# Kernel tuning notes

Measured on AMD Instinct MI355X. Metric: run time of the kernel, lower is better.

The kernel has to match this reference:

```python
import jax, jax.numpy as jnp
import numpy as np

WS = 3          # windows_size
ND = 3          # num_dilation, dilations [1,2,3]
NSTATE = 16     # d_state
RANK = 12       # dt_rank = ceil(192/16)
TOPK = 36       # max(1,(20//3)**2)*depth
DM = 192        # d_model
DI = 384        # d_inner = 2*d_model
B0, HH, WW = 8, 96, 96


def setup_inputs() -> dict:
    ks = jax.random.split(jax.random.key(0), 12)
    f = jax.random.normal
    return {
        "x": f(ks[0], (B0, HH, WW, DM), jnp.float32),
        "W_in": f(ks[1], (2 * DI, DM), jnp.float32) * 0.02,
        "conv_w": f(ks[2], (DI, 1, 7, 7), jnp.float32) * 0.05,
        "conv_b": f(ks[3], (DI,), jnp.float32) * 0.01,
        "x_proj_w": f(ks[4], (2, RANK + 2 * NSTATE, DI), jnp.float32) * 0.02,
        "dt_w": f(ks[5], (2, DI, RANK), jnp.float32) * 0.02,
        "dt_b": f(ks[6], (2, DI), jnp.float32) * 0.01,
        "A_logs": jnp.tile(jnp.log(jnp.arange(1, NSTATE + 1, dtype=jnp.float32)), (2 * DI, 1)),
        "Ds": jnp.ones((2 * DI,), jnp.float32),
        "W_kv": f(ks[7], (2 * DI, DI), jnp.float32) * 0.02,
        "b_kv": jnp.zeros((2 * DI,), jnp.float32),
        "ln_g": jnp.ones((DI,), jnp.float32),
        "ln_b": jnp.zeros((DI,), jnp.float32),
        "W_out": f(ks[8], (DM, DI), jnp.float32) * 0.02,
    }


def _selective_scan(xs, x_proj_w, dt_w, dt_b, A_logs, Ds):
    # xs: (B, K=2, D, L) -> (B, K, D, L). Standard Mamba selective scan.
    B, K, D, L = xs.shape
    x_dbl = jnp.einsum('bkdl,kcd->bkcl', xs, x_proj_w)          # (B,K,R+2N,L)
    dts = x_dbl[:, :, :RANK]
    Bs = x_dbl[:, :, RANK:RANK + NSTATE]                        # (B,K,N,L)
    Cs = x_dbl[:, :, RANK + NSTATE:]                            # (B,K,N,L)
    delta = jax.nn.softplus(jnp.einsum('bkrl,kdr->bkdl', dts, dt_w) + dt_b[None, :, :, None])
    A = -jnp.exp(A_logs).reshape(K, D, NSTATE)
    dA = jnp.exp(delta[..., None] * A[None, :, :, None, :])    # (B,K,D,L,N)
    dBu = delta[..., None] * Bs.transpose(0, 1, 3, 2)[:, :, None, :, :] * xs[..., None]
    dA = jnp.moveaxis(dA, 3, 0)                                 # (L,B,K,D,N)
    dBu = jnp.moveaxis(dBu, 3, 0)
    C = jnp.moveaxis(Cs, 3, 0)                                  # (L,B,K,N)

    def step(h, inp):
        dA_t, dBu_t, C_t = inp
        h = dA_t * h + dBu_t
        y = jnp.einsum('bkdn,bkn->bkd', h, C_t)
        return h, y

    h0 = jnp.zeros((B, K, D, NSTATE), xs.dtype)
    _, ys = jax.lax.scan(step, h0, (dA, dBu, C))                # ys: (L,B,K,D)
    y = jnp.moveaxis(ys, 0, 3)                                  # (B,K,D,L)
    return y + Ds.reshape(1, K, D, 1) * xs


def _dynamic_mask_active(x):
    # x: (B,D,H,W). Partition into WSxWS windows, keep TOPK by mean activation.
    B, D, H, W = x.shape
    nH, nW = H // WS, W // WS
    w = x.reshape(B, D, nH, WS, nW, WS).transpose(0, 2, 4, 1, 3, 5)
    w = w.reshape(B, nH * nW, D, WS * WS)                       # (B,nWin,D,ws2)
    score = w.mean(axis=(2, 3))                                 # (B,nWin)
    _, idx = jax.lax.top_k(score, TOPK)                         # (B,TOPK)
    g = jnp.take_along_axis(w, idx[:, :, None, None], axis=1)   # (B,TOPK,D,ws2)
    return g.transpose(0, 2, 1, 3).reshape(B, D, TOPK * WS * WS)


def _unfold(x, d):
    # torch nn.Unfold(kernel=WS, dilation=d, padding=d, stride=1) on (B,C,H,W)
    B, C, H, W = x.shape
    xp = jnp.pad(x, ((0, 0), (0, 0), (d, d), (d, d)))
    pats = [xp[:, :, i * d:i * d + H, j * d:j * d + W] for i in range(WS) for j in range(WS)]
    p = jnp.stack(pats, axis=2)                                 # (B,C,ws2,H,W) channel-major like torch
    return p.reshape(B, C, WS * WS, H * W)


def _forward(x, W_in, conv_w, conv_b, x_proj_w, dt_w, dt_b, A_logs, Ds,
             W_kv, b_kv, ln_g, ln_b, W_out):
    B, H, W_, _ = x.shape
    xz = jnp.einsum('bhwc,oc->bhwo', x, W_in)
    xf, z = jnp.split(xz, 2, axis=-1)                           # (B,H,W,DI) each
    xc = xf.transpose(0, 3, 1, 2)
    xc = jax.lax.conv_general_dilated(xc, conv_w, (1, 1), [(3, 3), (3, 3)],
                                      feature_group_count=conv_w.shape[0],
                                      dimension_numbers=('NCHW', 'OIHW', 'NCHW'))
    xc = xc + conv_b[None, :, None, None]                       # (B,DI,H,W)
    D = xc.shape[1]

    # foreground SSM on active windows (forward + flipped scan)
    act = _dynamic_mask_active(xc)                              # (B,D,L)
    xs = jnp.stack([act, jnp.flip(act, axis=-1)], axis=1)       # (B,2,D,L)
    out = _selective_scan(xs, x_proj_w, dt_w, dt_b, A_logs, Ds)
    y1 = out[:, 0] + jnp.flip(out[:, 1], axis=-1)               # (B,D,L)
    y1 = y1.transpose(0, 2, 1)                                  # (B,L,D)

    L = y1.shape[1]
    ws2 = WS * WS
    n2 = L // ws2
    kv = jnp.einsum('bld,od->blo', y1, W_kv) + b_kv             # (B,L,2D)
    hd = 2 * D // ND
    t = kv.reshape(B, n2, ws2, ND, hd).transpose(3, 0, 4, 2, 1)  # (ND,B,hd,ws2,n2)
    Q, Kt = t[:, :, :hd // 2], t[:, :, hd // 2:]                 # (ND,B,D/ND,ws2,n2)

    dch = D // ND
    xr = xc.reshape(B, ND, dch, H, W_)
    ys = []
    for i in range(ND):
        V = _unfold(xr[:, i], i + 1)                            # (B,dch,ws2,n1)
        V = V.transpose(0, 1, 3, 2)                             # (B,dch,n1,ws2)
        s = jnp.einsum('bcwn,bcwn->bcw', Q[i], Kt[i]) / np.sqrt(dch).astype(np.float32)
        # softmax over a singleton axis (as in the source) -> all ones
        A_M = jax.nn.softmax(s[..., None], axis=-1)[..., 0]     # (B,dch,ws2)
        ys.append(jnp.einsum('bcnw,bcw->bcn', V, A_M))          # (B,dch,n1)
    y = jnp.concatenate(ys, axis=1)                             # (B,D,n1)
    y = y.transpose(0, 2, 1)                                    # (B,n1,D)

    mu = y.mean(-1, keepdims=True)
    var = y.var(-1, keepdims=True)
    y = (y - mu) / jnp.sqrt(var + 1e-5) * ln_g + ln_b
    y = y.reshape(B, H, W_, D) + z
    return jnp.einsum('bhwd,od->bhwo', y, W_out)


def reference(x, W_in, conv_w, conv_b, x_proj_w, dt_w, dt_b, A_logs, Ds,
              W_kv, b_kv, ln_g, ln_b, W_out):
    return _forward(x, W_in, conv_w, conv_b, x_proj_w, dt_w, dt_b, A_logs, Ds,
                    W_kv, b_kv, ln_g, ln_b, W_out)
```

## Files before the change

kernel.cpp:

```cpp
#include <hip/hip_runtime.h>
#include <cstddef>

#define B0V 8
#define HSV 96
#define WSV 96
#define DMV 192
#define DIV 384
#define MTOT (B0V*HSV*WSV)

typedef __attribute__((ext_vector_type(8))) unsigned short ushort8v;
typedef __attribute__((ext_vector_type(8))) short short8v;
typedef __attribute__((ext_vector_type(4))) float f32x4;
typedef _Float16 h2 __attribute__((ext_vector_type(2)));
typedef _Float16 h8 __attribute__((ext_vector_type(8)));

__device__ __forceinline__ unsigned short f2bf(float f) {
    unsigned int i; __builtin_memcpy(&i, &f, 4);
    i += 0x7FFFu + ((i >> 16) & 1);
    return (unsigned short)(i >> 16);
}

template<int ROWS>
__device__ __forceinline__ void stageBF16(const unsigned short* __restrict__ src, int ld,
                                          unsigned short* lds, int t) {
#pragma unroll
    for (int i = 0; i < ROWS*8/256; ++i) {
        const int cid = t + i*256;
        const int r = cid >> 3, cb = cid & 7;
        ushort8v sv = *(const ushort8v*)(src + (size_t)r*ld + cb*8);
        *(ushort8v*)((char*)lds + r*128 + ((cb ^ (r&7))<<4)) = sv;
    }
}
__device__ __forceinline__ short8v fragRead(const unsigned short* lds, int row, int kchunk) {
    return *(const short8v*)((const char*)lds + row*128 + ((kchunk ^ (row&7))<<4));
}

__global__ __launch_bounds__(192) void wc_kernel(
    const float* __restrict__ Wout, const float* __restrict__ Win,
    unsigned short* __restrict__ Wch)
{
    const int o = blockIdx.x;
    const int c = threadIdx.x;
    __shared__ float wrow[384];
    for (int j = threadIdx.x; j < 384; j += 192) wrow[j] = Wout[(size_t)o*384 + j];
    __syncthreads();
    float acc = 0.f;
#pragma unroll 4
    for (int j = 0; j < 384; ++j)
        acc += wrow[j] * Win[(size_t)(384 + j)*192 + c];
    Wch[(size_t)o*192 + c] = f2bf(acc);
}

__global__ __launch_bounds__(256) void wprep_kernel(
    const float* __restrict__ cw, h2* __restrict__ w2h)
{
    const int idx = blockIdx.x*256 + threadIdx.x;
    if (idx < 49*192) {
        const int tap = idx / 192, cp = idx % 192;
        h2 v;
        v[0] = (_Float16)cw[(size_t)(2*cp  )*49 + tap];
        v[1] = (_Float16)cw[(size_t)(2*cp+1)*49 + tap];
        w2h[idx] = v;
    }
}

__global__ __launch_bounds__(256) void cvt_kernel(
    const float* __restrict__ src, unsigned short* __restrict__ dst, int n8)
{
    const int i = blockIdx.x*256 + threadIdx.x;
    if (i < n8) {
        const float4 f0 = *(const float4*)(src + (size_t)i*8);
        const float4 f1 = *(const float4*)(src + (size_t)i*8 + 4);
        ushort8v v;
        v[0]=f2bf(f0.x); v[1]=f2bf(f0.y); v[2]=f2bf(f0.z); v[3]=f2bf(f0.w);
        v[4]=f2bf(f1.x); v[5]=f2bf(f1.y); v[6]=f2bf(f1.z); v[7]=f2bf(f1.w);
        *(ushort8v*)(dst + (size_t)i*8) = v;
    }
}

__global__ __launch_bounds__(256) void gemm_in_mfma(
    const unsigned short* __restrict__ xh, const unsigned short* __restrict__ Wh,
    _Float16* __restrict__ xf)
{
    __shared__ unsigned short As[3*128*64];
    __shared__ unsigned short Bs[128*64];
    const int t = threadIdx.x;
    const int m0 = blockIdx.x * 128;
    const int wid = t >> 6, lane = t & 63;
    const int wm = wid >> 1, wn = wid & 1;
    const int li = lane & 15, lg = lane >> 4;

#pragma unroll
    for (int kb = 0; kb < 3; ++kb)
        stageBF16<128>(xh + (size_t)m0*DMV + kb*64, DMV, As + kb*128*64, t);

    for (int n0i = 0; n0i < 3; ++n0i) {
        const int n0 = n0i * 128;
        f32x4 acc[4][4];
#pragma unroll
        for (int i = 0; i < 4; ++i)
#pragma unroll
            for (int j = 0; j < 4; ++j) acc[i][j] = (f32x4){0.f,0.f,0.f,0.f};

        for (int kb = 0; kb < 3; ++kb) {
            __syncthreads();
            stageBF16<128>(Wh + (size_t)n0*DMV + kb*64, DMV, Bs, t);
            __syncthreads();
#pragma unroll
            for (int ks = 0; ks < 2; ++ks) {
                short8v a[4], b[4];
#pragma unroll
                for (int mf = 0; mf < 4; ++mf)
                    a[mf] = fragRead(As + kb*128*64, wm*64 + mf*16 + li, ks*4 + lg);
#pragma unroll
                for (int nf = 0; nf < 4; ++nf)
                    b[nf] = fragRead(Bs, wn*64 + nf*16 + li, ks*4 + lg);
#pragma unroll
                for (int mf = 0; mf < 4; ++mf)
#pragma unroll
                    for (int nf = 0; nf < 4; ++nf)
                        acc[mf][nf] = __builtin_amdgcn_mfma_f32_16x16x32_bf16(a[mf], b[nf], acc[mf][nf], 0, 0, 0);
            }
        }
#pragma unroll
        for (int mf = 0; mf < 4; ++mf)
#pragma unroll
            for (int nf = 0; nf < 4; ++nf)
#pragma unroll
                for (int i = 0; i < 4; ++i) {
                    const int row = m0 + wm*64 + mf*16 + lg*4 + i;
                    const int col = n0 + wn*64 + nf*16 + li;
                    xf[(size_t)row*DIV + col] = (_Float16)acc[mf][nf][i];
                }
    }
}

__global__ __launch_bounds__(256) void dwconv_kernel(
    const _Float16* __restrict__ xf, const h2* __restrict__ w2h,
    const float* __restrict__ cb, _Float16* __restrict__ xc)
{
    const int tile = blockIdx.x;
    const int th = tile / 6, tw = tile % 6;
    const int h0 = th*8, w0 = tw*16;
    const int c0 = blockIdx.y*64, b = blockIdx.z;

    __shared__ _Float16 patch[14*22*64];
    const int t = threadIdx.x;
    for (int idx = t; idx < 308*8; idx += 256) {
        const int sp = idx >> 3, c8 = idx & 7;
        const int ih = sp / 22, iw = sp - ih*22;
        const int gh = h0 - 3 + ih, gw = w0 - 3 + iw;
        ushort8v v;
#pragma unroll
        for (int j = 0; j < 8; ++j) v[j] = 0;
        if ((unsigned)gh < (unsigned)HSV && (unsigned)gw < (unsigned)WSV)
            v = *(const ushort8v*)(xf + (((size_t)b*HSV + gh)*WSV + gw)*DIV + c0 + c8*8);
        *(ushort8v*)(patch + sp*64 + c8*8) = v;
    }
    __syncthreads();

    const int cp = t & 31;
    const int wq = t >> 5;

    h2 wreg[49];
    const h2* wp = w2h + (c0 >> 1) + cp;
#pragma unroll
    for (int k = 0; k < 49; ++k) wreg[k] = wp[k*192];

    h2 biasv;
    biasv[0] = (_Float16)cb[c0 + 2*cp];
    biasv[1] = (_Float16)cb[c0 + 2*cp + 1];
    h2 acc[8][2];
#pragma unroll
    for (int i = 0; i < 8; ++i) { acc[i][0] = biasv; acc[i][1] = biasv; }

    const h2* prow = (const h2*)patch;
#pragma unroll
    for (int ih = 0; ih < 14; ++ih) {
        h2 r[8];
#pragma unroll
        for (int j = 0; j < 8; ++j)
            r[j] = prow[(ih*22 + wq*2 + j)*32 + cp];
#pragma unroll
        for (int kh = 0; kh < 7; ++kh) {
            const int oh = ih - kh;
            if (oh >= 0 && oh < 8) {
#pragma unroll
                for (int kw = 0; kw < 7; ++kw) {
                    acc[oh][0] += wreg[kh*7 + kw] * r[kw];
                    acc[oh][1] += wreg[kh*7 + kw] * r[kw + 1];
                }
            }
        }
    }
    h2* xcp = (h2*)xc;
#pragma unroll
    for (int oh = 0; oh < 8; ++oh)
#pragma unroll
        for (int j = 0; j < 2; ++j)
            xcp[((((size_t)b*HSV + h0+oh)*WSV + (w0 + wq*2 + j))*DIV + c0)/2 + cp] = acc[oh][j];
}

__global__ __launch_bounds__(256) void boxln_kernel(
    const _Float16* __restrict__ xc,
    const float* __restrict__ g, const float* __restrict__ bta,
    unsigned short* __restrict__ yln)
{
    const int wid  = threadIdx.x >> 6;
    const int lane = threadIdx.x & 63;
    const int m = blockIdx.x * 4 + wid;
    const int b  = m / (HSV*WSV);
    const int hw = m % (HSV*WSV);
    const int h = hw / WSV, w = hw % WSV;

    const bool act = lane < 48;
    const int ch = lane * 8;
    const int dd = (ch >> 7) + 1;

    float s[8];
#pragma unroll
    for (int j = 0; j < 8; ++j) s[j] = 0.f;

#pragma unroll
    for (int a = -1; a <= 1; ++a)
#pragma unroll
        for (int bb = -1; bb <= 1; ++bb) {
            const int h2_ = h + a*dd, w2_ = w + bb*dd;
            if (act && (unsigned)h2_ < (unsigned)HSV && (unsigned)w2_ < (unsigned)WSV) {
                h8 v = *(const h8*)(xc + (((size_t)b*HSV + h2_)*WSV + w2_)*DIV + ch);
#pragma unroll
                for (int j = 0; j < 8; ++j) s[j] += (float)v[j];
            }
        }

    float ps = 0.f, ps2 = 0.f;
#pragma unroll
    for (int j = 0; j < 8; ++j) { ps += s[j]; ps2 += s[j]*s[j]; }
#pragma unroll
    for (int off = 32; off > 0; off >>= 1) {
        ps  += __shfl_xor(ps,  off);
        ps2 += __shfl_xor(ps2, off);
    }
    const float mu   = ps * (1.f/384.f);
    const float var  = ps2 * (1.f/384.f) - mu*mu;
    const float rstd = rsqrtf(var + 1e-5f);

    if (act) {
        float4 g0 = *(const float4*)(g + ch);
        float4 g1 = *(const float4*)(g + ch + 4);
        float4 b0 = *(const float4*)(bta + ch);
        float4 b1 = *(const float4*)(bta + ch + 4);
        float gv[8] = {g0.x,g0.y,g0.z,g0.w,g1.x,g1.y,g1.z,g1.w};
        float bv[8] = {b0.x,b0.y,b0.z,b0.w,b1.x,b1.y,b1.z,b1.w};
        ushort8v o;
#pragma unroll
        for (int j = 0; j < 8; ++j)
            o[j] = f2bf((s[j] - mu)*rstd*gv[j] + bv[j]);
        *(ushort8v*)(yln + (size_t)m*DIV + ch) = o;
    }
}

__global__ __launch_bounds__(256) void gemm_out_mfma(
    const unsigned short* __restrict__ Yl, const unsigned short* __restrict__ WoutH,
    const unsigned short* __restrict__ xh, const unsigned short* __restrict__ Wch,
    float* __restrict__ out)
{
    __shared__ unsigned short As[128*64];
    __shared__ unsigned short Bs[192*64];
    const int t = threadIdx.x;
    const int m0 = blockIdx.x * 128;
    const int wid = t >> 6, lane = t & 63;
    const int wm = wid >> 1, wn = wid & 1;
    const int li = lane & 15, lg = lane >> 4;

    f32x4 acc[4][6];
#pragma unroll
    for (int i = 0; i < 4; ++i)
#pragma unroll
        for (int j = 0; j < 6; ++j) acc[i][j] = (f32x4){0.f,0.f,0.f,0.f};

    for (int kb = 0; kb < 9; ++kb) {
        if (kb < 6) {
            stageBF16<128>(Yl + (size_t)m0*DIV + kb*64, DIV, As, t);
            stageBF16<192>(WoutH + kb*64, DIV, Bs, t);
        } else {
            stageBF16<128>(xh + (size_t)m0*DMV + (kb-6)*64, DMV, As, t);
            stageBF16<192>(Wch + (kb-6)*64, DMV, Bs, t);
        }
        __syncthreads();
#pragma unroll
        for (int ks = 0; ks < 2; ++ks) {
            short8v a[4], b[6];
#pragma unroll
            for (int mf = 0; mf < 4; ++mf) a[mf] = fragRead(As, wm*64 + mf*16 + li, ks*4 + lg);
#pragma unroll
            for (int nf = 0; nf < 6; ++nf) b[nf] = fragRead(Bs, wn*96 + nf*16 + li, ks*4 + lg);
#pragma unroll
            for (int mf = 0; mf < 4; ++mf)
#pragma unroll
                for (int nf = 0; nf < 6; ++nf)
                    acc[mf][nf] = __builtin_amdgcn_mfma_f32_16x16x32_bf16(a[mf], b[nf], acc[mf][nf], 0, 0, 0);
        }
        __syncthreads();
    }
#pragma unroll
    for (int mf = 0; mf < 4; ++mf)
#pragma unroll
        for (int nf = 0; nf < 6; ++nf)
#pragma unroll
            for (int i = 0; i < 4; ++i) {
                const int row = m0 + wm*64 + mf*16 + lg*4 + i;
                const int col = wn*96 + nf*16 + li;
                out[(size_t)row*DMV + col] = acc[mf][nf][i];
            }
}

extern "C" void kernel_launch(void* const* d_in, const int* in_sizes, int n_in,
                              void* d_out, int out_size, void* d_ws, size_t ws_size,
                              hipStream_t stream)
{
    const float* x      = (const float*)d_in[0];
    const float* W_in   = (const float*)d_in[1];
    const float* conv_w = (const float*)d_in[2];
    const float* conv_b = (const float*)d_in[3];
    const float* ln_g   = (const float*)d_in[11];
    const float* ln_b   = (const float*)d_in[12];
    const float* W_out  = (const float*)d_in[13];
    float* out = (float*)d_out;

    char* ws = (char*)d_ws;
    unsigned short* Wch   = (unsigned short*)(ws);
    h2*             w2h   = (h2*)(ws + 0x20000);
    unsigned short* WinfH = (unsigned short*)(ws + 0x40000);
    unsigned short* WoutH = (unsigned short*)(ws + 0x80000);
    unsigned short* xh    = (unsigned short*)(ws + 0x100000);
    _Float16*       xf    = (_Float16*)(ws + 0x2000000);
    _Float16*       xc    = (_Float16*)d_out;

    wc_kernel    <<<dim3(192),              192, 0, stream>>>(W_out, W_in, Wch);
    wprep_kernel <<<dim3(37),               256, 0, stream>>>(conv_w, w2h);
    cvt_kernel   <<<dim3(36),               256, 0, stream>>>(W_in,  WinfH, 384*192/8);
    cvt_kernel   <<<dim3(36),               256, 0, stream>>>(W_out, WoutH, 192*384/8);
    cvt_kernel   <<<dim3(MTOT*DMV/8/256),   256, 0, stream>>>(x, xh, MTOT*DMV/8);
    gemm_in_mfma <<<dim3(MTOT/128),         256, 0, stream>>>(xh, WinfH, xf);
    dwconv_kernel<<<dim3(72, 6, B0V),       256, 0, stream>>>(xf, w2h, conv_b, xc);
    boxln_kernel <<<dim3(MTOT/4),           256, 0, stream>>>(xc, ln_g, ln_b,
                                                              (unsigned short*)xf);
    gemm_out_mfma<<<dim3(MTOT/128),         256, 0, stream>>>((const unsigned short*)xf,
                                                              WoutH, xh, Wch, out);
}
```

Before: 214.2 us.

## Fuse x bf16 conversion into input GEMM and widen dwconv tiles

The separate fp32-to-bf16 conversion kernel for x is removed. The input GEMM now loads fp32 x directly, converts it while staging into swizzled LDS, and also writes the bf16 copy that the output GEMM still needs. This saves one full pass that read x and wrote xh. Separately, the depthwise conv tile grows from 8x16 to 8x32, with each thread computing 4 output columns, so halo reloads shrink and register reuse improves, at the cost of more LDS and registers per block.

```diff
diff --git a/kernel.cpp b/kernel.cpp
--- a/kernel.cpp
+++ b/kernel.cpp
@@ -79,8 +79,8 @@
 }
 
 __global__ __launch_bounds__(256) void gemm_in_mfma(
-    const unsigned short* __restrict__ xh, const unsigned short* __restrict__ Wh,
-    _Float16* __restrict__ xf)
+    const float* __restrict__ x, const unsigned short* __restrict__ Wh,
+    unsigned short* __restrict__ xh, _Float16* __restrict__ xf)
 {
     __shared__ unsigned short As[3*128*64];
     __shared__ unsigned short Bs[128*64];
@@ -91,8 +91,21 @@
     const int li = lane & 15, lg = lane >> 4;
 
 #pragma unroll
-    for (int kb = 0; kb < 3; ++kb)
-        stageBF16<128>(xh + (size_t)m0*DMV + kb*64, DMV, As + kb*128*64, t);
+    for (int kb = 0; kb < 3; ++kb) {
+#pragma unroll
+        for (int i = 0; i < 4; ++i) {
+            const int cid = t + i*256;
+            const int r = cid >> 3, cb = cid & 7;
+            const float* p = x + (size_t)(m0 + r)*DMV + kb*64 + cb*8;
+            float4 f0 = *(const float4*)p;
+            float4 f1 = *(const float4*)(p+4);
+            ushort8v sv;
+            sv[0]=f2bf(f0.x); sv[1]=f2bf(f0.y); sv[2]=f2bf(f0.z); sv[3]=f2bf(f0.w);
+            sv[4]=f2bf(f1.x); sv[5]=f2bf(f1.y); sv[6]=f2bf(f1.z); sv[7]=f2bf(f1.w);
+            *(ushort8v*)((char*)(As + kb*128*64) + r*128 + ((cb ^ (r&7))<<4)) = sv;
+            *(ushort8v*)(xh + (size_t)(m0 + r)*DMV + kb*64 + cb*8) = sv;
+        }
+    }
 
     for (int n0i = 0; n0i < 3; ++n0i) {
         const int n0 = n0i * 128;
@@ -140,15 +153,15 @@
     const float* __restrict__ cb, _Float16* __restrict__ xc)
 {
     const int tile = blockIdx.x;
-    const int th = tile / 6, tw = tile % 6;
-    const int h0 = th*8, w0 = tw*16;
+    const int th = tile / 3, tw = tile % 3;
+    const int h0 = th*8, w0 = tw*32;
     const int c0 = blockIdx.y*64, b = blockIdx.z;
 
-    __shared__ _Float16 patch[14*22*64];
+    __shared__ _Float16 patch[14*38*64];
     const int t = threadIdx.x;
-    for (int idx = t; idx < 308*8; idx += 256) {
+    for (int idx = t; idx < 14*38*8; idx += 256) {
         const int sp = idx >> 3, c8 = idx & 7;
-        const int ih = sp / 22, iw = sp - ih*22;
+        const int ih = sp / 38, iw = sp - ih*38;
         const int gh = h0 - 3 + ih, gw = w0 - 3 + iw;
         ushort8v v;
 #pragma unroll
@@ -170,26 +183,28 @@
     h2 biasv;
     biasv[0] = (_Float16)cb[c0 + 2*cp];
     biasv[1] = (_Float16)cb[c0 + 2*cp + 1];
-    h2 acc[8][2];
-#pragma unroll
-    for (int i = 0; i < 8; ++i) { acc[i][0] = biasv; acc[i][1] = biasv; }
-
-    const h2* prow = (const h2*)patch;
+    h2 acc[8][4];
+#pragma unroll
+    for (int i = 0; i < 8; ++i)
+#pragma unroll
+        for (int j = 0; j < 4; ++j) acc[i][j] = biasv;
+
+    const h2* prow = (const h2*)patch + wq*4*32 + cp;
 #pragma unroll
     for (int ih = 0; ih < 14; ++ih) {
-        h2 r[8];
-#pragma unroll
-        for (int j = 0; j < 8; ++j)
-            r[j] = prow[(ih*22 + wq*2 + j)*32 + cp];
+        h2 r[10];
+#pragma unroll
+        for (int jj = 0; jj < 10; ++jj)
+            r[jj] = prow[(ih*38 + jj)*32];
 #pragma unroll
         for (int kh = 0; kh < 7; ++kh) {
             const int oh = ih - kh;
             if (oh >= 0 && oh < 8) {
 #pragma unroll
-                for (int kw = 0; kw < 7; ++kw) {
-                    acc[oh][0] += wreg[kh*7 + kw] * r[kw];
-                    acc[oh][1] += wreg[kh*7 + kw] * r[kw + 1];
-                }
+                for (int kw = 0; kw < 7; ++kw)
+#pragma unroll
+                    for (int j = 0; j < 4; ++j)
+                        acc[oh][j] += wreg[kh*7 + kw] * r[j + kw];
             }
         }
     }
@@ -197,8 +212,8 @@
 #pragma unroll
     for (int oh = 0; oh < 8; ++oh)
 #pragma unroll
-        for (int j = 0; j < 2; ++j)
-            xcp[((((size_t)b*HSV + h0+oh)*WSV + (w0 + wq*2 + j))*DIV + c0)/2 + cp] = acc[oh][j];
+        for (int j = 0; j < 4; ++j)
+            xcp[((((size_t)b*HSV + h0+oh)*WSV + (w0 + wq*4 + j))*DIV + c0)/2 + cp] = acc[oh][j];
 }
 
 __global__ __launch_bounds__(256) void boxln_kernel(
@@ -337,15 +352,14 @@
     _Float16*       xf    = (_Float16*)(ws + 0x2000000);
     _Float16*       xc    = (_Float16*)d_out;
 
-    wc_kernel    <<<dim3(192),              192, 0, stream>>>(W_out, W_in, Wch);
-    wprep_kernel <<<dim3(37),               256, 0, stream>>>(conv_w, w2h);
-    cvt_kernel   <<<dim3(36),               256, 0, stream>>>(W_in,  WinfH, 384*192/8);
-    cvt_kernel   <<<dim3(36),               256, 0, stream>>>(W_out, WoutH, 192*384/8);
-    cvt_kernel   <<<dim3(MTOT*DMV/8/256),   256, 0, stream>>>(x, xh, MTOT*DMV/8);
-    gemm_in_mfma <<<dim3(MTOT/128),         256, 0, stream>>>(xh, WinfH, xf);
-    dwconv_kernel<<<dim3(72, 6, B0V),       256, 0, stream>>>(xf, w2h, conv_b, xc);
-    boxln_kernel <<<dim3(MTOT/4),           256, 0, stream>>>(xc, ln_g, ln_b,
-                                                              (unsigned short*)xf);
-    gemm_out_mfma<<<dim3(MTOT/128),         256, 0, stream>>>((const unsigned short*)xf,
-                                                              WoutH, xh, Wch, out);
-}
+    wc_kernel    <<<dim3(192),          192, 0, stream>>>(W_out, W_in, Wch);
+    wprep_kernel <<<dim3(37),           256, 0, stream>>>(conv_w, w2h);
+    cvt_kernel   <<<dim3(36),           256, 0, stream>>>(W_in,  WinfH, 384*192/8);
+    cvt_kernel   <<<dim3(36),           256, 0, stream>>>(W_out, WoutH, 192*384/8);
+    gemm_in_mfma <<<dim3(MTOT/128),     256, 0, stream>>>(x, WinfH, xh, xf);
+    dwconv_kernel<<<dim3(36, 6, B0V),   256, 0, stream>>>(xf, w2h, conv_b, xc);
+    boxln_kernel <<<dim3(MTOT/4),       256, 0, stream>>>(xc, ln_g, ln_b,
+                                                          (unsigned short*)xf);
+    gemm_out_mfma<<<dim3(MTOT/128),     256, 0, stream>>>((const unsigned short*)xf,
+                                                          WoutH, xh, Wch, out);
+}
```

Result: no change. 216.4 us (+1.0%).
